# Optimization experiments

Hardware: AMD Instinct MI355X
Metric: run time of the kernel (lower is better)

The kernel has to match this reference:

```python
import jax, jax.numpy as jnp
import numpy as np

HIDDEN = 64
IN_DIM = 32
CONNECTION = 8
N_WARPS = (CONNECTION + 1) // 2  # range(0, connection, 2) -> 4 warps actually used


def conv2d(x, w, b, pad):
    # x: (B, Cin, H, W), w: (Cout, Cin, kh, kw)
    y = jax.lax.conv_general_dilated(
        x, w, window_strides=(1, 1), padding=[(pad, pad), (pad, pad)],
        dimension_numbers=("NCHW", "OIHW", "NCHW"))
    return y + b[None, :, None, None]


def grid_sample_bilinear(img, grid):
    """torch.nn.functional.grid_sample(mode='bilinear', padding_mode='zeros', align_corners=False).
    img: (B, C, H, W); grid: (B, H, W, 2) with grid[..., 0]=x (width), grid[..., 1]=y (height)."""
    B, C, H, W = img.shape
    gx = (grid[..., 0] + 1.0) * (W * 0.5) - 0.5  # unnormalize, align_corners=False
    gy = (grid[..., 1] + 1.0) * (H * 0.5) - 0.5
    x0 = jnp.floor(gx)
    y0 = jnp.floor(gy)
    wx1 = gx - x0
    wy1 = gy - y0
    wx0 = 1.0 - wx1
    wy0 = 1.0 - wy1

    def gather(xf, yf):
        valid = (xf >= 0) & (xf < W) & (yf >= 0) & (yf < H)
        xi = jnp.clip(xf, 0, W - 1).astype(jnp.int32)
        yi = jnp.clip(yf, 0, H - 1).astype(jnp.int32)
        # per-batch advanced gather: (C, H, W) per sample
        v = jax.vmap(lambda im, y, x: im[:, y, x])(img, yi, xi)  # (B, C, H, W)
        return v * valid[:, None, :, :].astype(img.dtype)

    out = (wy0 * wx0)[:, None] * gather(x0, y0) \
        + (wy0 * wx1)[:, None] * gather(x0 + 1, y0) \
        + (wy1 * wx0)[:, None] * gather(x0, y0 + 1) \
        + (wy1 * wx1)[:, None] * gather(x0 + 1, y0 + 1)
    return out


def setup_inputs() -> dict:
    key = jax.random.key(0)
    ks = jax.random.split(key, 10)
    B, H, W = 16, 128, 128
    s = 0.05
    return {
        "x": jax.random.normal(ks[0], (B, IN_DIM, H, W), dtype=jnp.float32),
        "h_prev": jax.random.normal(ks[1], (B, HIDDEN, H, W), dtype=jnp.float32),
        "w_in": jax.random.normal(ks[2], (3 * HIDDEN, IN_DIM, 3, 3), dtype=jnp.float32) * s,
        "b_in": jax.random.normal(ks[3], (3 * HIDDEN,), dtype=jnp.float32) * s,
        "w_proj": jax.random.normal(ks[4], (N_WARPS, 3 * HIDDEN, HIDDEN), dtype=jnp.float32) * s,
        "b_proj": jax.random.normal(ks[5], (N_WARPS, 3 * HIDDEN), dtype=jnp.float32) * s,
        "w_sub": jax.random.normal(ks[6], (2 * CONNECTION, IN_DIM + HIDDEN, 5, 5), dtype=jnp.float32) * s,
        "b_sub": jax.random.normal(ks[7], (2 * CONNECTION,), dtype=jnp.float32) * s,
    }


def reference(x, h_prev, w_in, b_in, w_proj, b_proj, w_sub, b_sub):
    d = HIDDEN
    input_conv = conv2d(x, w_in, b_in, pad=1)  # (B, 3d, H, W)
    x_z, x_r, x_h = input_conv[:, :d], input_conv[:, d:2 * d], input_conv[:, 2 * d:]

    # flow sub-network + global min-max normalization over ALL channels
    combined = jnp.concatenate([x, h_prev], axis=1)
    cc = conv2d(combined, w_sub, b_sub, pad=2)  # (B, 2*connection, H, W)
    cc = jnp.transpose(cc, (0, 2, 3, 1))        # (B, H, W, 2*connection)
    cc = (cc - cc.min()) / (cc.max() - cc.min())
    cc = 2.0 * cc - 1.0

    traj = None
    for i in range(N_WARPS):  # small fixed loop (mirrors range(0, connection, 2))
        grid = cc[..., 2 * i:2 * i + 2]
        warped = grid_sample_bilinear(h_prev, grid)  # (B, d, H, W)
        proj = jnp.einsum("bchw,oc->bohw", warped, w_proj[i]) + b_proj[i][None, :, None, None]
        traj = proj if traj is None else traj + proj

    h_z, h_r, h_h = traj[:, :d], traj[:, d:2 * d], traj[:, 2 * d:]
    z = jax.nn.sigmoid(x_z + h_z)
    r = jax.nn.sigmoid(x_r + h_r)
    h = jax.nn.leaky_relu(x_h + r * h_h, negative_slope=0.2)
    h_next = (1.0 - z) * h + z * h_prev
    return h_next
```

## Files before the change

kernel.cpp:

```cpp
#include <hip/hip_runtime.h>
#include <hip/hip_bf16.h>
#include <math.h>

#define B_    16
#define HID   64
#define CIN   32
#define OC1   192
#define CCC   16
#define HW_   128
#define NPIX  (HW_*HW_)

typedef _Float16 half8 __attribute__((ext_vector_type(8)));
typedef float floatx4 __attribute__((ext_vector_type(4)));

__device__ __forceinline__ unsigned fenc(float f) {
    unsigned b = __float_as_uint(f);
    return (b & 0x80000000u) ? ~b : (b | 0x80000000u);
}
__device__ __forceinline__ float fdec(unsigned u) {
    unsigned b = (u & 0x80000000u) ? (u ^ 0x80000000u) : ~u;
    return __uint_as_float(b);
}

__global__ __launch_bounds__(256) void repack_kernel(
    const float* __restrict__ w_in, const float* __restrict__ w_sub,
    const float* __restrict__ w_proj, const float* __restrict__ b_proj,
    _Float16* __restrict__ wsub_f16, float* __restrict__ bsum,
    _Float16* __restrict__ win_f16, _Float16* __restrict__ wp_f16,
    unsigned* __restrict__ minmax)
{
    int idx = blockIdx.x * 256 + threadIdx.x;
    if (idx < 38400) {
        int sk = idx >> 9, r2 = idx & 511;
        int l = r2 >> 3, j = r2 & 7;
        int s = sk / 3, kc = sk - s * 3;
        int ky = s / 5, kx = s - ky * 5;
        int oc = l & 15;
        int icg = kc * 32 + (l >> 4) * 8 + j;
        wsub_f16[idx] = (_Float16)w_sub[oc * 2400 + icg * 25 + ky * 5 + kx];
    } else if (idx < 38400 + 192) {
        int o = idx - 38400;
        bsum[o] = b_proj[o] + b_proj[192 + o] + b_proj[384 + o] + b_proj[576 + o];
    } else if (idx < 38592 + 55296) {
        int j2 = idx - 38592;
        int s = j2 / 6144, r = j2 - s * 6144;
        int mt = r / 512, r2 = r - mt * 512;
        int l = r2 >> 3, j = r2 & 7;
        int oc = mt * 16 + (l & 15);
        int ic = (l >> 4) * 8 + j;
        win_f16[j2] = (_Float16)w_in[oc * 288 + ic * 9 + s];
    } else if (idx < 38592 + 55296 + 49152) {
        int j3 = idx - (38592 + 55296);
        int kt = j3 / 6144, r = j3 - kt * 6144;
        int mt = r / 512, r2 = r - mt * 512;
        int l = r2 >> 3, j = r2 & 7;
        int o = mt * 16 + (l & 15);
        int c_all = kt * 32 + (l >> 4) * 8 + j;
        int i = c_all >> 6, c = c_all & 63;
        wp_f16[j3] = (_Float16)w_proj[(i * 192 + o) * 64 + c];
    }
    if (idx == 0) { minmax[0] = 0xFFFFFFFFu; minmax[1] = 0u; }
}

__global__ __launch_bounds__(256) void transpose_h_kernel(
    const float* __restrict__ hp, const float* __restrict__ x,
    _Float16* __restrict__ hcl, _Float16* __restrict__ xcl)
{
    __shared__ float lds[64 * 129];
    int tid = threadIdx.x;
    int y = blockIdx.x, b = blockIdx.y;

    const float* hb = hp + (size_t)b * HID * NPIX + y * HW_;
#pragma unroll
    for (int it = 0; it < 32; ++it) {
        int idx = tid + it * 256;
        int c = idx >> 7, xx = idx & 127;
        lds[c * 129 + xx] = hb[(size_t)c * NPIX + xx];
    }
    __syncthreads();
    unsigned* o = (unsigned*)(hcl + (size_t)((b * HW_ + y) * HW_) * 64);
#pragma unroll
    for (int it = 0; it < 16; ++it) {
        int e2 = tid + it * 256;
        int c2 = e2 & 31, xx = e2 >> 5;
        union { _Float16 h[2]; unsigned u; } pk;
        pk.h[0] = (_Float16)lds[(c2 * 2) * 129 + xx];
        pk.h[1] = (_Float16)lds[(c2 * 2 + 1) * 129 + xx];
        o[e2] = pk.u;
    }
    __syncthreads();

    const float* xb = x + (size_t)b * CIN * NPIX + y * HW_;
#pragma unroll
    for (int it = 0; it < 16; ++it) {
        int idx = tid + it * 256;
        int c = idx >> 7, xx = idx & 127;
        lds[c * 129 + xx] = xb[(size_t)c * NPIX + xx];
    }
    __syncthreads();
    unsigned* ox = (unsigned*)(xcl + (size_t)((b * HW_ + y) * HW_) * 32);
#pragma unroll
    for (int it = 0; it < 8; ++it) {
        int e2 = tid + it * 256;
        int c2 = e2 & 15, xx = e2 >> 4;
        union { _Float16 h[2]; unsigned u; } pk;
        pk.h[0] = (_Float16)lds[(c2 * 2) * 129 + xx];
        pk.h[1] = (_Float16)lds[(c2 * 2 + 1) * 129 + xx];
        ox[e2] = pk.u;
    }
}

__global__ __launch_bounds__(256) void conv_sub_mfma(
    const _Float16* __restrict__ xcl, const _Float16* __restrict__ hcl,
    const _Float16* __restrict__ wsub_f16, const float* __restrict__ b_sub,
    float* __restrict__ cc, unsigned* __restrict__ minmax)
{
    __shared__ __align__(16) _Float16 tile[12 * 20 * 104];
    __shared__ float redmn[4], redmx[4];
    int tid = threadIdx.x;
    int b = blockIdx.z;
    int y0 = blockIdx.y * 8, x0 = blockIdx.x * 16;

#pragma unroll
    for (int it = 0; it < 8; ++it) {
        int idx = tid + it * 256;
        if (idx < 1920) {
            int yy = idx / 160, rem = idx - yy * 160;
            int px = rem >> 3, q = rem & 7;
            int gy = y0 + yy - 2, gx = x0 + px - 2;
            bool ok = ((unsigned)gy < 128u) & ((unsigned)gx < 128u);
            int cgy = min(max(gy, 0), 127), cgx = min(max(gx, 0), 127);
            uint4 v = ((const uint4*)hcl)[(size_t)((b * 128 + cgy) * 128 + cgx) * 8 + q];
            if (!ok) { v.x = 0; v.y = 0; v.z = 0; v.w = 0; }
            *(uint4*)((char*)tile + (yy * 20 + px) * 208 + 64 + q * 16) = v;
        }
    }
#pragma unroll
    for (int it = 0; it < 4; ++it) {
        int idx = tid + it * 256;
        if (idx < 960) {
            int yy = idx / 80, rem = idx - yy * 80;
            int px = rem >> 2, q = rem & 3;
            int gy = y0 + yy - 2, gx = x0 + px - 2;
            bool ok = ((unsigned)gy < 128u) & ((unsigned)gx < 128u);
            int cgy = min(max(gy, 0), 127), cgx = min(max(gx, 0), 127);
            uint4 v = ((const uint4*)xcl)[(size_t)((b * 128 + cgy) * 128 + cgx) * 4 + q];
            if (!ok) { v.x = 0; v.y = 0; v.z = 0; v.w = 0; }
            *(uint4*)((char*)tile + (yy * 20 + px) * 208 + q * 16) = v;
        }
    }
    __syncthreads();

    int w = tid >> 6, l = tid & 63;
    int quad = l >> 4, ln = l & 15;

    floatx4 sinit;
#pragma unroll
    for (int r = 0; r < 4; ++r) sinit[r] = b_sub[quad * 4 + r];
    floatx4 sacc[2] = {sinit, sinit};

#pragma unroll 5
    for (int s = 0; s < 25; ++s) {
        int ky = s / 5, kx = s - (s / 5) * 5;
#pragma unroll
        for (int kc = 0; kc < 3; ++kc) {
            half8 af = *(const half8*)(wsub_f16 + (size_t)((s * 3 + kc) * 64 + l) * 8);
#pragma unroll
            for (int t = 0; t < 2; ++t) {
                int pos = (w * 2 + t + ky) * 20 + (ln + kx);
                half8 bf = *(const half8*)(tile + pos * 104 + kc * 32 + quad * 8);
                sacc[t] = __builtin_amdgcn_mfma_f32_16x16x32_f16(af, bf, sacc[t], 0, 0, 0);
            }
        }
    }

    {
        float mn = 1e30f, mx = -1e30f;
#pragma unroll
        for (int t = 0; t < 2; ++t) {
            int yg = y0 + w * 2 + t;
#pragma unroll
            for (int r = 0; r < 4; ++r) {
                int oc = quad * 4 + r;
                float v = sacc[t][r];
                cc[((size_t)(b * CCC + oc) * HW_ + yg) * HW_ + x0 + ln] = v;
                mn = fminf(mn, v); mx = fmaxf(mx, v);
            }
        }
#pragma unroll
        for (int m = 1; m < 64; m <<= 1) {
            mn = fminf(mn, __shfl_xor(mn, m, 64));
            mx = fmaxf(mx, __shfl_xor(mx, m, 64));
        }
        if (l == 0) { redmn[w] = mn; redmx[w] = mx; }
    }
    __syncthreads();
    if (tid == 0) {
        float bmn = fminf(fminf(redmn[0], redmn[1]), fminf(redmn[2], redmn[3]));
        float bmx = fmaxf(fmaxf(redmx[0], redmx[1]), fmaxf(redmx[2], redmx[3]));
        atomicMin(&minmax[0], fenc(bmn));
        atomicMax(&minmax[1], fenc(bmx));
    }
}

__global__ __launch_bounds__(256, 3) void warp_gru_conv(
    const float* __restrict__ hp, const _Float16* __restrict__ hcl,
    const _Float16* __restrict__ xcl, const float* __restrict__ cc,
    const _Float16* __restrict__ wp_f16, const float* __restrict__ bsum,
    const _Float16* __restrict__ win_f16, const float* __restrict__ b_in,
    const unsigned* __restrict__ minmax, float* __restrict__ out)
{
    __shared__ __align__(16) _Float16 warped[64 * 256];
    __shared__ __align__(16) _Float16 xt[3 * 72 * 32];
    int tid = threadIdx.x;
    int i = tid >> 6;
    int p = tid & 63;
    int b = blockIdx.z, y = blockIdx.y, xh = blockIdx.x;
    int xg = xh * 64 + p;
    int w = i, l = p;
    int quad = l >> 4, ln = l & 15;

    uint4 xv0, xv1, xv2, xv3;
    int xslot = -1;
    if (tid < 216) {
        int row = tid / 72, px = tid - row * 72;
        int gy = y - 1 + row, gx = xh * 64 - 4 + px;
        bool ok = ((unsigned)gy < 128u) & ((unsigned)gx < 128u);
        int cgy = min(max(gy, 0), 127), cgx = min(max(gx, 0), 127);
        const uint4* s = (const uint4*)(xcl + (size_t)((b * 128 + cgy) * 128 + cgx) * 32);
        xv0 = s[0]; xv1 = s[1]; xv2 = s[2]; xv3 = s[3];
        if (!ok) {
            xv0.x = xv0.y = xv0.z = xv0.w = 0; xv1 = xv0; xv2 = xv0; xv3 = xv0;
        }
        xslot = (row * 72 + px) * 4;
    }

    float mn = fdec(minmax[0]), mx = fdec(minmax[1]);
    float scale = 2.0f / (mx - mn);
    int ccbase = ((b * CCC + 2 * i) * HW_ + y) * HW_ + xg;
    float gxn = (cc[ccbase] - mn) * scale - 1.0f;
    float gyn = (cc[ccbase + NPIX] - mn) * scale - 1.0f;
    float gx = (gxn + 1.0f) * 64.0f - 0.5f;
    float gy = (gyn + 1.0f) * 64.0f - 0.5f;
    float x0f = floorf(gx), y0f = floorf(gy);
    float wx1 = gx - x0f, wy1 = gy - y0f;
    float wx0 = 1.0f - wx1, wy0 = 1.0f - wy1;
    int ix0 = (int)x0f, iy0 = (int)y0f;
    int ix1 = ix0 + 1, iy1 = iy0 + 1;
    bool vx0 = (unsigned)ix0 < 128u, vx1 = (unsigned)ix1 < 128u;
    bool vy0 = (unsigned)iy0 < 128u, vy1 = (unsigned)iy1 < 128u;
    float a00 = (vx0 && vy0) ? wy0 * wx0 : 0.f;
    float a01 = (vx1 && vy0) ? wy0 * wx1 : 0.f;
    float a10 = (vx0 && vy1) ? wy1 * wx0 : 0.f;
    float a11 = (vx1 && vy1) ? wy1 * wx1 : 0.f;
    int cx0 = min(max(ix0, 0), 127), cx1 = min(max(ix1, 0), 127);
    int cy0 = min(max(iy0, 0), 127), cy1 = min(max(iy1, 0), 127);

    const _Float16* hclb = hcl + (size_t)b * NPIX * 64;
    const half8* r00 = (const half8*)(hclb + (size_t)(cy0 * HW_ + cx0) * 64);
    const half8* r01 = (const half8*)(hclb + (size_t)(cy0 * HW_ + cx1) * 64);
    const half8* r10 = (const half8*)(hclb + (size_t)(cy1 * HW_ + cx0) * 64);
    const half8* r11 = (const half8*)(hclb + (size_t)(cy1 * HW_ + cx1) * 64);

#pragma unroll
    for (int t = 0; t < 8; ++t) {
        half8 c00 = r00[t], c01 = r01[t], c10 = r10[t], c11 = r11[t];
        half8 pk;
#pragma unroll
        for (int e = 0; e < 8; ++e) {
            float v = a00 * (float)c00[e] + a01 * (float)c01[e]
                    + a10 * (float)c10[e] + a11 * (float)c11[e];
            pk[e] = (_Float16)v;
        }
        int cs = (i * 8 + t) ^ (p & 7);
        *(half8*)(warped + p * 256 + cs * 8) = pk;
    }

    if (xslot >= 0) {
        unsigned b0 = (unsigned)(xslot * 16);
        unsigned by0_ = b0 ^ (((b0 >> 7) & 3) << 4);
        unsigned b1 = (unsigned)((xslot + 1) * 16);
        unsigned by1_ = b1 ^ (((b1 >> 7) & 3) << 4);
        unsigned b2 = (unsigned)((xslot + 2) * 16);
        unsigned by2_ = b2 ^ (((b2 >> 7) & 3) << 4);
        unsigned b3 = (unsigned)((xslot + 3) * 16);
        unsigned by3_ = b3 ^ (((b3 >> 7) & 3) << 4);
        *(uint4*)((char*)xt + by0_) = xv0;
        *(uint4*)((char*)xt + by1_) = xv1;
        *(uint4*)((char*)xt + by2_) = xv2;
        *(uint4*)((char*)xt + by3_) = xv3;
    }
    __syncthreads();

    const float* hb = hp + (size_t)b * HID * NPIX;
    float hpv[4][4];
#pragma unroll
    for (int nt = 0; nt < 4; ++nt) {
#pragma unroll
        for (int r = 0; r < 4; ++r) {
            int d = 16 * w + quad * 4 + r;
            hpv[nt][r] = hb[(size_t)d * NPIX + y * HW_ + xh * 64 + nt * 16 + ln];
        }
    }

    floatx4 iacc[3][4];
#pragma unroll
    for (int t = 0; t < 3; ++t) {
        floatx4 bi = *(const floatx4*)(b_in + t * 64 + 16 * w + quad * 4);
#pragma unroll
        for (int nt = 0; nt < 4; ++nt) iacc[t][nt] = bi;
    }
#pragma unroll
    for (int s = 0; s < 9; ++s) {
        int ky = s / 3, kx = s - ky * 3;
        half8 af[3];
#pragma unroll
        for (int t = 0; t < 3; ++t)
            af[t] = *(const half8*)(win_f16 + (size_t)((s * 12 + (t * 4 + w)) * 64 + l) * 8);
#pragma unroll
        for (int nt = 0; nt < 4; ++nt) {
            int pxr = ky * 72 + nt * 16 + ln + kx + 3;
            unsigned byte = (unsigned)(pxr * 64 + quad * 16);
            byte ^= ((byte >> 7) & 3) << 4;
            half8 bf = *(const half8*)((char*)xt + byte);
#pragma unroll
            for (int t = 0; t < 3; ++t)
                iacc[t][nt] = __builtin_amdgcn_mfma_f32_16x16x32_f16(af[t], bf, iacc[t][nt], 0, 0, 0);
        }
    }

    floatx4 acc[3][4];
#pragma unroll
    for (int t = 0; t < 3; ++t) {
        floatx4 bs = *(const floatx4*)(bsum + t * 64 + 16 * w + quad * 4);
#pragma unroll
        for (int nt = 0; nt < 4; ++nt) acc[t][nt] = bs;
    }
#pragma unroll
    for (int kt = 0; kt < 8; ++kt) {
        half8 af[3];
#pragma unroll
        for (int t = 0; t < 3; ++t)
            af[t] = *(const half8*)(wp_f16 + (size_t)((kt * 12 + (t * 4 + w)) * 64 + l) * 8);
#pragma unroll
        for (int nt = 0; nt < 4; ++nt) {
            int pxi = nt * 16 + ln;
            int cs = (kt * 4 + quad) ^ (pxi & 7);
            half8 bf = *(const half8*)(warped + pxi * 256 + cs * 8);
#pragma unroll
            for (int t = 0; t < 3; ++t)
                acc[t][nt] = __builtin_amdgcn_mfma_f32_16x16x32_f16(af[t], bf, acc[t][nt], 0, 0, 0);
        }
    }

#pragma unroll
    for (int nt = 0; nt < 4; ++nt) {
#pragma unroll
        for (int r = 0; r < 4; ++r) {
            int d = 16 * w + quad * 4 + r;
            int pxi = nt * 16 + ln;
            int pix = y * HW_ + xh * 64 + pxi;
            float z  = 1.0f / (1.0f + expf(-(iacc[0][nt][r] + acc[0][nt][r])));
            float rg = 1.0f / (1.0f + expf(-(iacc[1][nt][r] + acc[1][nt][r])));
            float hc = iacc[2][nt][r] + rg * acc[2][nt][r];
            hc = hc > 0.f ? hc : 0.2f * hc;
            out[(size_t)(b * HID + d) * NPIX + pix] = (1.f - z) * hc + z * hpv[nt][r];
        }
    }
}

extern "C" void kernel_launch(void* const* d_in, const int* in_sizes, int n_in,
                              void* d_out, int out_size, void* d_ws, size_t ws_size,
                              hipStream_t stream)
{
    const float* x      = (const float*)d_in[0];
    const float* hp     = (const float*)d_in[1];
    const float* w_in   = (const float*)d_in[2];
    const float* b_in   = (const float*)d_in[3];
    const float* w_proj = (const float*)d_in[4];
    const float* b_proj = (const float*)d_in[5];
    const float* w_sub  = (const float*)d_in[6];
    const float* b_sub  = (const float*)d_in[7];
    float* out = (float*)d_out;

    char* ws = (char*)d_ws;
    float*     ccbuf    = (float*)    ws;
    unsigned*  minmax   = (unsigned*) (ws + 16777216);
    _Float16*  wsub_f16 = (_Float16*)(ws + 16777472);
    float*     bsum     = (float*)    (ws + 16854272);
    _Float16*  win_f16  = (_Float16*)(ws + 16855296);
    _Float16*  wp_f16   = (_Float16*)(ws + 16965888);
    _Float16*  hcl16    = (_Float16*)(ws + 17064192);
    _Float16*  xcl16    = (_Float16*)(ws + 50618624);

    repack_kernel<<<dim3(559), dim3(256), 0, stream>>>(
        w_in, w_sub, w_proj, b_proj, wsub_f16, bsum, win_f16, wp_f16, minmax);
    transpose_h_kernel<<<dim3(HW_, B_), dim3(256), 0, stream>>>(hp, x, hcl16, xcl16);
    conv_sub_mfma<<<dim3(8, 16, B_), dim3(256), 0, stream>>>(
        xcl16, hcl16, wsub_f16, b_sub, ccbuf, minmax);
    warp_gru_conv<<<dim3(2, HW_, B_), dim3(256), 0, stream>>>(
        hp, hcl16, xcl16, ccbuf, wp_f16, bsum, win_f16, b_in, minmax, out);
}
```

Before: 395.6 us.

## Alias LDS buffers, merge z/r accumulators, and raise occupancy of fused GRU kernel

The fused warp+GRU kernel now reuses one shared buffer for the input-conv tile and the warped features, moving the bilinear gather after the input conv and adding extra barriers between the phases. The z and r gate accumulators of the input conv and the projection are merged into one set, which cuts accumulator registers. The bilinear interpolation is done in packed fp16 instead of fp32, and fast exp replaces expf. Launch bounds are raised to 4 blocks per CU to increase occupancy. The cost is that the gather loads are no longer overlapped with the conv, and fp16 interpolation loses some precision.

```diff
diff --git a/kernel.cpp b/kernel.cpp
--- a/kernel.cpp
+++ b/kernel.cpp
@@ -203,15 +203,17 @@
     }
 }
 
-__global__ __launch_bounds__(256, 3) void warp_gru_conv(
+__global__ __launch_bounds__(256, 4) void warp_gru_conv(
     const float* __restrict__ hp, const _Float16* __restrict__ hcl,
     const _Float16* __restrict__ xcl, const float* __restrict__ cc,
     const _Float16* __restrict__ wp_f16, const float* __restrict__ bsum,
     const _Float16* __restrict__ win_f16, const float* __restrict__ b_in,
     const unsigned* __restrict__ minmax, float* __restrict__ out)
 {
-    __shared__ __align__(16) _Float16 warped[64 * 256];
-    __shared__ __align__(16) _Float16 xt[3 * 72 * 32];
+    __shared__ __align__(16) _Float16 smem[64 * 256];
+    _Float16* xt = smem;
+    _Float16* warped = smem;
+
     int tid = threadIdx.x;
     int i = tid >> 6;
     int p = tid & 63;
@@ -249,10 +251,10 @@
     int ix1 = ix0 + 1, iy1 = iy0 + 1;
     bool vx0 = (unsigned)ix0 < 128u, vx1 = (unsigned)ix1 < 128u;
     bool vy0 = (unsigned)iy0 < 128u, vy1 = (unsigned)iy1 < 128u;
-    float a00 = (vx0 && vy0) ? wy0 * wx0 : 0.f;
-    float a01 = (vx1 && vy0) ? wy0 * wx1 : 0.f;
-    float a10 = (vx0 && vy1) ? wy1 * wx0 : 0.f;
-    float a11 = (vx1 && vy1) ? wy1 * wx1 : 0.f;
+    _Float16 h00 = (_Float16)((vx0 && vy0) ? wy0 * wx0 : 0.f);
+    _Float16 h01 = (_Float16)((vx1 && vy0) ? wy0 * wx1 : 0.f);
+    _Float16 h10 = (_Float16)((vx0 && vy1) ? wy1 * wx0 : 0.f);
+    _Float16 h11 = (_Float16)((vx1 && vy1) ? wy1 * wx1 : 0.f);
     int cx0 = min(max(ix0, 0), 127), cx1 = min(max(ix1, 0), 127);
     int cy0 = min(max(iy0, 0), 127), cy1 = min(max(iy1, 0), 127);
 
@@ -261,20 +263,6 @@
     const half8* r01 = (const half8*)(hclb + (size_t)(cy0 * HW_ + cx1) * 64);
     const half8* r10 = (const half8*)(hclb + (size_t)(cy1 * HW_ + cx0) * 64);
     const half8* r11 = (const half8*)(hclb + (size_t)(cy1 * HW_ + cx1) * 64);
-
-#pragma unroll
-    for (int t = 0; t < 8; ++t) {
-        half8 c00 = r00[t], c01 = r01[t], c10 = r10[t], c11 = r11[t];
-        half8 pk;
-#pragma unroll
-        for (int e = 0; e < 8; ++e) {
-            float v = a00 * (float)c00[e] + a01 * (float)c01[e]
-                    + a10 * (float)c10[e] + a11 * (float)c11[e];
-            pk[e] = (_Float16)v;
-        }
-        int cs = (i * 8 + t) ^ (p & 7);
-        *(half8*)(warped + p * 256 + cs * 8) = pk;
-    }
 
     if (xslot >= 0) {
         unsigned b0 = (unsigned)(xslot * 16);
@@ -292,24 +280,25 @@
     }
     __syncthreads();
 
-    const float* hb = hp + (size_t)b * HID * NPIX;
-    float hpv[4][4];
-#pragma unroll
-    for (int nt = 0; nt < 4; ++nt) {
-#pragma unroll
-        for (int r = 0; r < 4; ++r) {
-            int d = 16 * w + quad * 4 + r;
-            hpv[nt][r] = hb[(size_t)d * NPIX + y * HW_ + xh * 64 + nt * 16 + ln];
-        }
-    }
-
-    floatx4 iacc[3][4];
-#pragma unroll
-    for (int t = 0; t < 3; ++t) {
+    floatx4 accA[3][4];
+    floatx4 hh[4];
+#pragma unroll
+    for (int t = 0; t < 2; ++t) {
         floatx4 bi = *(const floatx4*)(b_in + t * 64 + 16 * w + quad * 4);
-#pragma unroll
-        for (int nt = 0; nt < 4; ++nt) iacc[t][nt] = bi;
-    }
+        floatx4 bs = *(const floatx4*)(bsum + t * 64 + 16 * w + quad * 4);
+        floatx4 init;
+#pragma unroll
+        for (int r = 0; r < 4; ++r) init[r] = bi[r] + bs[r];
+#pragma unroll
+        for (int nt = 0; nt < 4; ++nt) accA[t][nt] = init;
+    }
+    {
+        floatx4 bih = *(const floatx4*)(b_in + 128 + 16 * w + quad * 4);
+        floatx4 bsh = *(const floatx4*)(bsum + 128 + 16 * w + quad * 4);
+#pragma unroll
+        for (int nt = 0; nt < 4; ++nt) { accA[2][nt] = bih; hh[nt] = bsh; }
+    }
+
 #pragma unroll
     for (int s = 0; s < 9; ++s) {
         int ky = s / 3, kx = s - ky * 3;
@@ -325,17 +314,31 @@
             half8 bf = *(const half8*)((char*)xt + byte);
 #pragma unroll
             for (int t = 0; t < 3; ++t)
-                iacc[t][nt] = __builtin_amdgcn_mfma_f32_16x16x32_f16(af[t], bf, iacc[t][nt], 0, 0, 0);
-        }
-    }
-
-    floatx4 acc[3][4];
-#pragma unroll
-    for (int t = 0; t < 3; ++t) {
-        floatx4 bs = *(const floatx4*)(bsum + t * 64 + 16 * w + quad * 4);
-#pragma unroll
-        for (int nt = 0; nt < 4; ++nt) acc[t][nt] = bs;
-    }
+                accA[t][nt] = __builtin_amdgcn_mfma_f32_16x16x32_f16(af[t], bf, accA[t][nt], 0, 0, 0);
+        }
+    }
+    __syncthreads();
+
+#pragma unroll
+    for (int t = 0; t < 8; ++t) {
+        half8 c00 = r00[t], c01 = r01[t], c10 = r10[t], c11 = r11[t];
+        half8 v = c00 * h00 + c01 * h01 + c10 * h10 + c11 * h11;
+        int cs = (i * 8 + t) ^ (p & 7);
+        *(half8*)(warped + p * 256 + cs * 8) = v;
+    }
+    __syncthreads();
+
+    const float* hb = hp + (size_t)b * HID * NPIX;
+    float hpv[4][4];
+#pragma unroll
+    for (int nt = 0; nt < 4; ++nt) {
+#pragma unroll
+        for (int r = 0; r < 4; ++r) {
+            int d = 16 * w + quad * 4 + r;
+            hpv[nt][r] = hb[(size_t)d * NPIX + y * HW_ + xh * 64 + nt * 16 + ln];
+        }
+    }
+
 #pragma unroll
     for (int kt = 0; kt < 8; ++kt) {
         half8 af[3];
@@ -347,9 +350,9 @@
             int pxi = nt * 16 + ln;
             int cs = (kt * 4 + quad) ^ (pxi & 7);
             half8 bf = *(const half8*)(warped + pxi * 256 + cs * 8);
-#pragma unroll
-            for (int t = 0; t < 3; ++t)
-                acc[t][nt] = __builtin_amdgcn_mfma_f32_16x16x32_f16(af[t], bf, acc[t][nt], 0, 0, 0);
+            accA[0][nt] = __builtin_amdgcn_mfma_f32_16x16x32_f16(af[0], bf, accA[0][nt], 0, 0, 0);
+            accA[1][nt] = __builtin_amdgcn_mfma_f32_16x16x32_f16(af[1], bf, accA[1][nt], 0, 0, 0);
+            hh[nt]      = __builtin_amdgcn_mfma_f32_16x16x32_f16(af[2], bf, hh[nt], 0, 0, 0);
         }
     }
 
@@ -360,9 +363,9 @@
             int d = 16 * w + quad * 4 + r;
             int pxi = nt * 16 + ln;
             int pix = y * HW_ + xh * 64 + pxi;
-            float z  = 1.0f / (1.0f + expf(-(iacc[0][nt][r] + acc[0][nt][r])));
-            float rg = 1.0f / (1.0f + expf(-(iacc[1][nt][r] + acc[1][nt][r])));
-            float hc = iacc[2][nt][r] + rg * acc[2][nt][r];
+            float z  = 1.0f / (1.0f + __expf(-accA[0][nt][r]));
+            float rg = 1.0f / (1.0f + __expf(-accA[1][nt][r]));
+            float hc = accA[2][nt][r] + rg * hh[nt][r];
             hc = hc > 0.f ? hc : 0.2f * hc;
             out[(size_t)(b * HID + d) * NPIX + pix] = (1.f - z) * hc + z * hpv[nt][r];
         }
```

After: 393.9 us. Within noise of the previous version (-0.4%).
